# Kernel optimization log

Measured on AMD Instinct MI355X. Metric: run time of the kernel, lower is better.

The kernel has to match this reference:

```python
import jax, jax.numpy as jnp
from jax import lax
import numpy as np

B, N, NPOINT, NSAMPLE, C = 4, 8192, 2048, 32, 128
RADIUS = 0.2
H1, H2, OUT = 64, 128, 128  # mlp: (3+C)->H1->H2, sas: H2->OUT


def fps(xyz, npoint):
    # furthest point sampling: xyz (B,N,3) -> idx (B,npoint) int32
    b, n, _ = xyz.shape
    init_idx = jnp.zeros((b,), jnp.int32)

    def step(carry, _):
        dist, last = carry
        p = jnp.take_along_axis(xyz, last[:, None, None], axis=1)  # (B,1,3)
        d = jnp.sum((xyz - p) ** 2, axis=-1)                       # (B,N)
        dist = jnp.minimum(dist, d)
        nxt = jnp.argmax(dist, axis=-1).astype(jnp.int32)
        return (dist, nxt), nxt

    (_, _), rest = lax.scan(step, (jnp.full((b, n), 1e10, jnp.float32), init_idx),
                            None, length=npoint - 1)
    return jnp.concatenate([init_idx[None, :], rest], axis=0).T    # (B,npoint)


def ball_query(xyz, new_xyz, radius, nsample):
    # xyz (B,N,3), new_xyz (B,S,3) -> idx (B,S,nsample) int32
    n = xyz.shape[1]
    d2 = jnp.sum((new_xyz[:, :, None, :] - xyz[:, None, :, :]) ** 2, axis=-1)  # (B,S,N)
    ar = jnp.arange(n, dtype=jnp.int32)
    keys = jnp.where(d2 <= radius * radius, ar, n)  # valid -> own index, invalid -> N
    neg_vals, _ = lax.top_k(-keys, nsample)          # smallest nsample keys
    idx = -neg_vals
    first = idx[..., :1]
    return jnp.where(idx >= n, first, idx)           # pad invalid with first valid


def gather_points(pts, idx):
    # pts (B,N,D), idx (B,S,ns) -> (B,S,ns,D)
    b, s, ns = idx.shape
    flat = jnp.take_along_axis(pts, idx.reshape(b, s * ns, 1), axis=1)
    return flat.reshape(b, s, ns, -1)


def setup_inputs() -> dict:
    key = jax.random.key(0)
    ks = jax.random.split(key, 8)
    xyz = jax.random.uniform(ks[0], (B, N, 3), dtype=jnp.float32)
    features = jax.random.normal(ks[1], (B, C, N), dtype=jnp.float32)
    cin = C + 3
    W1 = jax.random.normal(ks[2], (H1, cin), dtype=jnp.float32) / np.sqrt(cin)
    b1 = jnp.zeros((H1,), jnp.float32)
    W2 = jax.random.normal(ks[3], (H2, H1), dtype=jnp.float32) / np.sqrt(H1)
    b2 = jnp.zeros((H2,), jnp.float32)
    Wsa = jax.random.normal(ks[4], (OUT, H2), dtype=jnp.float32) / np.sqrt(H2)
    bsa = jnp.zeros((OUT,), jnp.float32)
    return {"xyz": xyz, "features": features, "W1": W1, "b1": b1,
            "W2": W2, "b2": b2, "Wsa": Wsa, "bsa": bsa}


def reference(xyz, features, W1, b1, W2, b2, Wsa, bsa):
    center_idx = fps(xyz, NPOINT)                                   # (B,S)
    new_xyz = jnp.take_along_axis(xyz, center_idx[:, :, None], axis=1)  # (B,S,3)
    g_idx = ball_query(xyz, new_xyz, RADIUS, NSAMPLE)               # (B,S,ns)
    g_xyz = gather_points(xyz, g_idx) - new_xyz[:, :, None, :]      # (B,S,ns,3) relative coords
    g_feat = gather_points(features.transpose(0, 2, 1), g_idx)      # (B,S,ns,C)
    h = jnp.concatenate([g_xyz, g_feat], axis=-1)                   # (B,S,ns,3+C)
    h = jax.nn.relu(jnp.einsum('bsnc,oc->bsno', h, W1) + b1)        # shared 1x1-conv MLP
    h = jax.nn.relu(jnp.einsum('bsnc,oc->bsno', h, W2) + b2)
    pooled = jnp.max(h, axis=2)                                     # max over nsample -> (B,S,H2)
    out = jnp.einsum('bsc,oc->bso', pooled, Wsa) + bsa              # sas channel mixer
    return new_xyz, out.transpose(0, 2, 1)                          # (B,S,3), (B,OUT,S)
```

## Files before the change

kernel.cpp:

```cpp
#include <hip/hip_runtime.h>
#include <cstdint>
#include <cstddef>

#define NB 4
#define NN 8192
#define NPTS 2048
#define NSAMP 32
#define NC 128
#define CIN 131
#define NH1 64
#define NH2 128
#define NOUTC 128
#define GCELLS 4096

typedef float v2f __attribute__((ext_vector_type(2)));

__device__ __forceinline__ float d2_exact(float ax, float ay, float az,
                                          float bx, float by, float bz) {
  float dx = ax - bx, dy = ay - by, dz = az - bz;
  return __fadd_rn(__fadd_rn(__fmul_rn(dx, dx), __fmul_rn(dy, dy)),
                   __fmul_rn(dz, dz));
}

#if __has_builtin(__builtin_amdgcn_mov_dpp)
template <int CTRL>
__device__ __forceinline__ float dppf(float v) {
  return __int_as_float(
      __builtin_amdgcn_mov_dpp(__float_as_int(v), CTRL, 0xF, 0xF, true));
}
template <int CTRL>
__device__ __forceinline__ int dppi(int v) {
  return __builtin_amdgcn_mov_dpp(v, CTRL, 0xF, 0xF, true);
}
#else
template <int CTRL>
__device__ __forceinline__ float dppf(float v) {
  const int m = (CTRL == 0xB1) ? 1 : (CTRL == 0x4E) ? 2 : (CTRL == 0x141) ? 7 : 15;
  return __shfl_xor(v, m);
}
template <int CTRL>
__device__ __forceinline__ int dppi(int v) {
  const int m = (CTRL == 0xB1) ? 1 : (CTRL == 0x4E) ? 2 : (CTRL == 0x141) ? 7 : 15;
  return __shfl_xor(v, m);
}
#endif

__device__ __forceinline__ bool tgt(float av, int ai, float bv, int bi) {
  return (av > bv) || (av == bv && ai < bi);
}

__device__ __forceinline__ void red_pair(float& bv, int& bi, float ov, int oi) {
  bool t = tgt(ov, oi, bv, bi);
  bv = t ? ov : bv;
  bi = t ? oi : bi;
}
template <int CTRL>
__device__ __forceinline__ void red5(float& v, int& i, float& x, float& y,
                                     float& z) {
  float ov = dppf<CTRL>(v);
  int oi = dppi<CTRL>(i);
  float ox = dppf<CTRL>(x), oy = dppf<CTRL>(y), oz = dppf<CTRL>(z);
  bool t = tgt(ov, oi, v, i);
  v = t ? ov : v; i = t ? oi : i;
  x = t ? ox : x; y = t ? oy : y; z = t ? oz : z;
}

#define SEL8(A, kk, out)                      \
  {                                           \
    float s0_ = ((kk) & 1) ? A[1] : A[0];     \
    float s1_ = ((kk) & 1) ? A[3] : A[2];     \
    float s2_ = ((kk) & 1) ? A[5] : A[4];     \
    float s3_ = ((kk) & 1) ? A[7] : A[6];     \
    float s4_ = ((kk) & 2) ? s1_ : s0_;       \
    float s5_ = ((kk) & 2) ? s3_ : s2_;       \
    out = ((kk) & 4) ? s5_ : s4_;             \
  }

__device__ __forceinline__ int spread3(int v) {
  return (v & 1) | ((v & 2) << 2) | ((v & 4) << 4) | ((v & 8) << 6);
}

__global__ __launch_bounds__(1024, 1) void sort_kernel(
    const float* __restrict__ xyz, float* __restrict__ xs,
    float* __restrict__ ys, float* __restrict__ zs, int* __restrict__ io) {
  __shared__ int hist[GCELLS];
  __shared__ int cbase[GCELLS];
  __shared__ int wtot[16];
  __shared__ int woff[16];
  const int b = blockIdx.x;
  const int tid = threadIdx.x;
  const int lane = tid & 63;
  const int wid = tid >> 6;
  const float* xb = xyz + (size_t)b * NN * 3;
  for (int i = tid; i < GCELLS; i += 1024) hist[i] = 0;
  __syncthreads();
  int cell[8];
  float px[8], py[8], pz[8];
#pragma unroll
  for (int k = 0; k < 8; ++k) {
    int j = tid + (k << 10);
    float x = xb[j * 3 + 0], y = xb[j * 3 + 1], z = xb[j * 3 + 2];
    px[k] = x; py[k] = y; pz[k] = z;
    int cx = min(15, max(0, (int)(x * 16.0f)));
    int cy = min(15, max(0, (int)(y * 16.0f)));
    int cz = min(15, max(0, (int)(z * 16.0f)));
    cell[k] = spread3(cx) | (spread3(cy) << 1) | (spread3(cz) << 2);
    atomicAdd(&hist[cell[k]], 1);
  }
  __syncthreads();
  const int i0 = tid * 4;
  int h0 = hist[i0], h1 = hist[i0 + 1], h2 = hist[i0 + 2], h3 = hist[i0 + 3];
  int s4 = h0 + h1 + h2 + h3;
  int v = s4;
#pragma unroll
  for (int d = 1; d < 64; d <<= 1) {
    int o = __shfl_up(v, d);
    if (lane >= d) v += o;
  }
  if (lane == 63) wtot[wid] = v;
  __syncthreads();
  if (tid < 16) {
    int acc = 0;
    for (int w = 0; w < 16; ++w) {
      if (w == tid) woff[tid] = acc;
      acc += wtot[w];
    }
  }
  __syncthreads();
  int eb = woff[wid] + v - s4;
  cbase[i0] = eb;
  cbase[i0 + 1] = eb + h0;
  cbase[i0 + 2] = eb + h0 + h1;
  cbase[i0 + 3] = eb + h0 + h1 + h2;
  __syncthreads();
  for (int i = tid; i < GCELLS; i += 1024) hist[i] = 0;
  __syncthreads();
  const size_t bo = (size_t)b * NN;
#pragma unroll
  for (int k = 0; k < 8; ++k) {
    int pos = cbase[cell[k]] + atomicAdd(&hist[cell[k]], 1);
    xs[bo + pos] = px[k];
    ys[bo + pos] = py[k];
    zs[bo + pos] = pz[k];
    io[bo + pos] = tid + (k << 10);
  }
}

__global__ __launch_bounds__(1024, 1) void fps_kernel(
    const float* __restrict__ xyz, const float* __restrict__ xs,
    const float* __restrict__ ys, const float* __restrict__ zs,
    const int* __restrict__ io, float* __restrict__ newxyz) {
#pragma clang fp contract(off)
  const int b = blockIdx.x;
  const int tid = threadIdx.x;
  const int lane = tid & 63;
  const int wid = tid >> 6;
  const size_t bo = (size_t)b * NN;

  float X[8], Y[8], Z[8], D[8];
  int I[8];
#pragma unroll
  for (int k = 0; k < 8; ++k) {
    int s = tid * 8 + k;
    X[k] = xs[bo + s];
    Y[k] = ys[bo + s];
    Z[k] = zs[bo + s];
    I[k] = io[bo + s];
    D[k] = 1e30f;
  }

  __shared__ float sv[16];
  __shared__ int si[16];
  __shared__ float sx[16], sy[16], sz[16];
  __shared__ float fin[3];

  const float* xb = xyz + (size_t)b * NN * 3;
  float cx = xb[0], cy = xb[1], cz = xb[2];
  if (tid == 0) {
    newxyz[(size_t)b * NPTS * 3 + 0] = cx;
    newxyz[(size_t)b * NPTS * 3 + 1] = cy;
    newxyz[(size_t)b * NPTS * 3 + 2] = cz;
  }

  for (int t = 1; t < NPTS; ++t) {
    float bv = -1.0f;
    int bi = 0x7fffffff;
    int kw = 0;
#pragma unroll
    for (int k = 0; k < 8; ++k) {
      float dd = d2_exact(X[k], Y[k], Z[k], cx, cy, cz);
      float nd = fminf(D[k], dd);
      D[k] = nd;
      bool c = tgt(nd, I[k], bv, bi);
      bv = c ? nd : bv;
      bi = c ? I[k] : bi;
      kw = c ? k : kw;
    }
    float rv = bv;
    int ri = bi;
    red_pair(rv, ri, dppf<0xB1>(rv), dppi<0xB1>(ri));
    red_pair(rv, ri, dppf<0x4E>(rv), dppi<0x4E>(ri));
    red_pair(rv, ri, dppf<0x141>(rv), dppi<0x141>(ri));
    red_pair(rv, ri, dppf<0x140>(rv), dppi<0x140>(ri));
    red_pair(rv, ri, __shfl_xor(rv, 16), __shfl_xor(ri, 16));
    red_pair(rv, ri, __shfl_xor(rv, 32), __shfl_xor(ri, 32));
    if (bi == ri) {
      float ox, oy, oz;
      SEL8(X, kw, ox);
      SEL8(Y, kw, oy);
      SEL8(Z, kw, oz);
      sv[wid] = rv;
      si[wid] = ri;
      sx[wid] = ox;
      sy[wid] = oy;
      sz[wid] = oz;
    }
    __syncthreads();
    if (wid == 0) {
      const int e = lane & 15;
      float v = sv[e];
      int i = si[e];
      float xx = sx[e], yy = sy[e], zz = sz[e];
      red5<0xB1>(v, i, xx, yy, zz);
      red5<0x4E>(v, i, xx, yy, zz);
      red5<0x141>(v, i, xx, yy, zz);
      red5<0x140>(v, i, xx, yy, zz);
      if (lane == 0) {
        fin[0] = xx;
        fin[1] = yy;
        fin[2] = zz;
        size_t o = ((size_t)b * NPTS + t) * 3;
        newxyz[o + 0] = xx;
        newxyz[o + 1] = yy;
        newxyz[o + 2] = zz;
      }
    }
    __syncthreads();
    cx = fin[0];
    cy = fin[1];
    cz = fin[2];
  }
}

__global__ __launch_bounds__(1024, 1) void fps_nosort_kernel(
    const float* __restrict__ xyz, float* __restrict__ newxyz) {
#pragma clang fp contract(off)
  const int b = blockIdx.x;
  const int tid = threadIdx.x;
  const int lane = tid & 63;
  const int wid = tid >> 6;
  const float* xb = xyz + (size_t)b * NN * 3;
  v2f x2[4], y2[4], z2[4], dd[4];
#pragma unroll
  for (int p = 0; p < 4; ++p) {
    int j0 = tid + ((2 * p) << 10);
    int j1 = tid + ((2 * p + 1) << 10);
    x2[p].x = xb[j0 * 3 + 0]; x2[p].y = xb[j1 * 3 + 0];
    y2[p].x = xb[j0 * 3 + 1]; y2[p].y = xb[j1 * 3 + 1];
    z2[p].x = xb[j0 * 3 + 2]; z2[p].y = xb[j1 * 3 + 2];
    dd[p].x = 1e10f; dd[p].y = 1e10f;
  }
  __shared__ float vbuf[2][16];
  __shared__ int ibuf[2][16];
  __shared__ float cbuf[2][16][3];
  float cx = xb[0], cy = xb[1], cz = xb[2];
  if (tid == 0) {
    newxyz[(size_t)b * NPTS * 3 + 0] = cx;
    newxyz[(size_t)b * NPTS * 3 + 1] = cy;
    newxyz[(size_t)b * NPTS * 3 + 2] = cz;
  }
  for (int t = 1; t < NPTS; ++t) {
    const int par = t & 1;
    float bv = -1.0f; int bi = 0;
    float bwx = 0.f, bwy = 0.f, bwz = 0.f;
#pragma unroll
    for (int p = 0; p < 4; ++p) {
      v2f dx = x2[p] - (v2f){cx, cx};
      v2f dy = y2[p] - (v2f){cy, cy};
      v2f dz = z2[p] - (v2f){cz, cz};
      v2f s = dx * dx + dy * dy + dz * dz;
      v2f nd;
      nd.x = fminf(dd[p].x, s.x);
      nd.y = fminf(dd[p].y, s.y);
      dd[p] = nd;
      { bool c = nd.x > bv;
        bv = c ? nd.x : bv; bi = c ? (tid + ((2 * p) << 10)) : bi;
        bwx = c ? x2[p].x : bwx; bwy = c ? y2[p].x : bwy; bwz = c ? z2[p].x : bwz; }
      { bool c = nd.y > bv;
        bv = c ? nd.y : bv; bi = c ? (tid + ((2 * p + 1) << 10)) : bi;
        bwx = c ? x2[p].y : bwx; bwy = c ? y2[p].y : bwy; bwz = c ? z2[p].y : bwz; }
    }
    red_pair(bv, bi, dppf<0xB1>(bv), dppi<0xB1>(bi));
    red_pair(bv, bi, dppf<0x4E>(bv), dppi<0x4E>(bi));
    red_pair(bv, bi, dppf<0x141>(bv), dppi<0x141>(bi));
    red_pair(bv, bi, dppf<0x140>(bv), dppi<0x140>(bi));
    red_pair(bv, bi, __shfl_xor(bv, 16), __shfl_xor(bi, 16));
    red_pair(bv, bi, __shfl_xor(bv, 32), __shfl_xor(bi, 32));
    if (tid == (bi & 1023)) {
      vbuf[par][wid] = bv; ibuf[par][wid] = bi;
      cbuf[par][wid][0] = bwx; cbuf[par][wid][1] = bwy; cbuf[par][wid][2] = bwz;
    }
    __syncthreads();
    float v2w = vbuf[par][lane & 15];
    int i2w = ibuf[par][lane & 15];
    red_pair(v2w, i2w, dppf<0xB1>(v2w), dppi<0xB1>(i2w));
    red_pair(v2w, i2w, dppf<0x4E>(v2w), dppi<0x4E>(i2w));
    red_pair(v2w, i2w, dppf<0x141>(v2w), dppi<0x141>(i2w));
    red_pair(v2w, i2w, dppf<0x140>(v2w), dppi<0x140>(i2w));
    const int slot = (i2w & 1023) >> 6;
    cx = cbuf[par][slot][0]; cy = cbuf[par][slot][1]; cz = cbuf[par][slot][2];
    if (tid == (i2w & 1023)) {
      size_t o = ((size_t)b * NPTS + t) * 3;
      newxyz[o + 0] = cx; newxyz[o + 1] = cy; newxyz[o + 2] = cz;
    }
  }
}

__global__ __launch_bounds__(256) void ballq_kernel(
    const float* __restrict__ xyz, const float* __restrict__ newxyz,
    int* __restrict__ bidx) {
  const int cid = blockIdx.x * 4 + (threadIdx.x >> 6);
  const int lane = threadIdx.x & 63;
  const int b = cid >> 11;
  const float* xb = xyz + (size_t)b * NN * 3;
  const float cx = newxyz[(size_t)cid * 3 + 0];
  const float cy = newxyz[(size_t)cid * 3 + 1];
  const float cz = newxyz[(size_t)cid * 3 + 2];
  int* ob = bidx + (size_t)cid * NSAMP;
  int total = 0;
  int first = -1;
  for (int c0 = 0; c0 < NN; c0 += 64) {
    int j = c0 + lane;
    float xx = xb[j * 3 + 0], yy = xb[j * 3 + 1], zz = xb[j * 3 + 2];
    float d2 = d2_exact(cx, cy, cz, xx, yy, zz);
    bool in = d2 <= 0.04f;
    unsigned long long m = __ballot(in);
    if (first < 0 && m) first = c0 + __builtin_ctzll(m);
    int pos = total + __popcll(m & ((1ull << lane) - 1ull));
    if (in && pos < NSAMP) ob[pos] = j;
    total += __popcll(m);
    if (total >= NSAMP) break;
  }
  if (total < NSAMP && lane < NSAMP - total) ob[total + lane] = first;
}

__global__ void tw_kernel(const float* __restrict__ W1, const float* __restrict__ W2,
                          const float* __restrict__ Wsa, float* __restrict__ w1t,
                          float* __restrict__ w2t, float* __restrict__ wsat) {
  int i = blockIdx.x * blockDim.x + threadIdx.x;
  if (i < CIN * NH1) w1t[i] = W1[(i % NH1) * CIN + (i / NH1)];
  if (i < NH1 * NH2) w2t[i] = W2[(i % NH2) * NH1 + (i / NH2)];
  if (i < NH2 * NOUTC) wsat[i] = Wsa[(i % NOUTC) * NH2 + (i / NOUTC)];
}

__global__ void tfeat_kernel(const float* __restrict__ feat, float* __restrict__ featT) {
  __shared__ float tile[32][33];
  const int b = blockIdx.z;
  const int n0 = blockIdx.x * 32, c0 = blockIdx.y * 32;
  const int tx = threadIdx.x, ty = threadIdx.y;
#pragma unroll
  for (int r = 0; r < 4; ++r)
    tile[ty + r * 8][tx] = feat[((size_t)b * NC + c0 + ty + r * 8) * NN + n0 + tx];
  __syncthreads();
#pragma unroll
  for (int r = 0; r < 4; ++r)
    featT[((size_t)b * NN + n0 + ty + r * 8) * NC + c0 + tx] = tile[tx][ty + r * 8];
}

#define HS 36
__global__ __launch_bounds__(256) void mlp_kernel(
    const float* __restrict__ xyz, const float* __restrict__ fsrc,
    const float* __restrict__ newxyz, const int* __restrict__ bidx,
    const float* __restrict__ w1t, const float* __restrict__ b1,
    const float* __restrict__ w2t, const float* __restrict__ b2,
    const float* __restrict__ wsat, const float* __restrict__ bsa,
    float* __restrict__ out1, int useT) {
  __shared__ float h[CIN * HS];
  __shared__ float h1[NH1 * HS];
  __shared__ float pl[256];
  __shared__ float pooled[NH2];
  __shared__ int sidx[NSAMP];
  __shared__ float sc[3];
  const int cid = blockIdx.x;
  const int b = cid >> 11;
  const int s = cid & 2047;
  const int tid = threadIdx.x;
  if (tid < NSAMP) sidx[tid] = bidx[(size_t)cid * NSAMP + tid];
  if (tid < 3) sc[tid] = newxyz[(size_t)cid * 3 + tid];
  __syncthreads();
  {
    const int ss = tid >> 3, q = tid & 7;
    const int j = sidx[ss];
    if (useT) {
      const float4* fr = (const float4*)(fsrc + ((size_t)b * NN + j) * NC + q * 16);
#pragma unroll
      for (int u = 0; u < 4; ++u) {
        float4 v = fr[u];
        int c = 3 + q * 16 + u * 4;
        h[(c + 0) * HS + ss] = v.x;
        h[(c + 1) * HS + ss] = v.y;
        h[(c + 2) * HS + ss] = v.z;
        h[(c + 3) * HS + ss] = v.w;
      }
    } else {
      for (int u = 0; u < 16; ++u) {
        int c = q * 16 + u;
        h[(3 + c) * HS + ss] = fsrc[((size_t)b * NC + c) * NN + j];
      }
    }
    if (q == 0) {
      const float* pr = xyz + ((size_t)b * NN + j) * 3;
      h[0 * HS + ss] = pr[0] - sc[0];
      h[1 * HS + ss] = pr[1] - sc[1];
      h[2 * HS + ss] = pr[2] - sc[2];
    }
  }
  __syncthreads();
  {
    const int o = tid & 63, sg = tid >> 6;
    float acc[8];
    const float bb = b1[o];
#pragma unroll
    for (int i = 0; i < 8; ++i) acc[i] = bb;
    const float4* hb = (const float4*)&h[sg * 8];
    for (int k = 0; k < CIN; ++k) {
      float w = w1t[k * NH1 + o];
      float4 a = hb[k * (HS / 4) + 0];
      float4 c = hb[k * (HS / 4) + 1];
      acc[0] = fmaf(w, a.x, acc[0]); acc[1] = fmaf(w, a.y, acc[1]);
      acc[2] = fmaf(w, a.z, acc[2]); acc[3] = fmaf(w, a.w, acc[3]);
      acc[4] = fmaf(w, c.x, acc[4]); acc[5] = fmaf(w, c.y, acc[5]);
      acc[6] = fmaf(w, c.z, acc[6]); acc[7] = fmaf(w, c.w, acc[7]);
    }
#pragma unroll
    for (int i = 0; i < 8; ++i) h1[o * HS + sg * 8 + i] = fmaxf(acc[i], 0.0f);
  }
  __syncthreads();
  {
    const int o = tid & 127, sg = tid >> 7;
    float acc[16];
    const float bb = b2[o];
#pragma unroll
    for (int i = 0; i < 16; ++i) acc[i] = bb;
    const float4* hb = (const float4*)&h1[sg * 16];
    for (int k = 0; k < NH1; ++k) {
      float w = w2t[k * NH2 + o];
#pragma unroll
      for (int u = 0; u < 4; ++u) {
        float4 a = hb[k * (HS / 4) + u];
        acc[u * 4 + 0] = fmaf(w, a.x, acc[u * 4 + 0]);
        acc[u * 4 + 1] = fmaf(w, a.y, acc[u * 4 + 1]);
        acc[u * 4 + 2] = fmaf(w, a.z, acc[u * 4 + 2]);
        acc[u * 4 + 3] = fmaf(w, a.w, acc[u * 4 + 3]);
      }
    }
    float pm = acc[0];
#pragma unroll
    for (int i = 1; i < 16; ++i) pm = fmaxf(pm, acc[i]);
    pl[sg * 128 + o] = pm;
  }
  __syncthreads();
  if (tid < NH2) pooled[tid] = fmaxf(fmaxf(pl[tid], pl[128 + tid]), 0.0f);
  __syncthreads();
  if (tid < NOUTC) {
    float acc = bsa[tid];
    for (int k = 0; k < NH2; ++k) acc = fmaf(pooled[k], wsat[k * NOUTC + tid], acc);
    out1[((size_t)b * NOUTC + tid) * NPTS + s] = acc;
  }
}

extern "C" void kernel_launch(void* const* d_in, const int* in_sizes, int n_in,
                              void* d_out, int out_size, void* d_ws, size_t ws_size,
                              hipStream_t stream) {
  const float* xyz = (const float*)d_in[0];
  const float* feat = (const float*)d_in[1];
  const float* W1 = (const float*)d_in[2];
  const float* b1 = (const float*)d_in[3];
  const float* W2 = (const float*)d_in[4];
  const float* b2 = (const float*)d_in[5];
  const float* Wsa = (const float*)d_in[6];
  const float* bsa = (const float*)d_in[7];
  float* out = (float*)d_out;
  float* newxyz = out;
  float* out1 = out + (size_t)NB * NPTS * 3;

  const size_t sort_f = (size_t)NB * NN * 4;
  const size_t small_f = (size_t)CIN * NH1 + NH1 * NH2 + NH2 * NOUTC +
                         (size_t)NB * NPTS * NSAMP;
  const size_t featT_f = (size_t)NB * NN * NC;

  float* ws = (float*)d_ws;
  bool useSort = ws_size >= (sort_f + small_f) * 4;
  bool useT = ws_size >= (sort_f + small_f + featT_f) * 4;

  float* xs = ws;
  float* ysr = xs + (size_t)NB * NN;
  float* zsr = ysr + (size_t)NB * NN;
  int* iosr = (int*)(zsr + (size_t)NB * NN);
  float* base2 = useSort ? (ws + sort_f) : ws;
  float* w1t = base2;
  float* w2t = w1t + CIN * NH1;
  float* wsat = w2t + NH1 * NH2;
  int* bidx = (int*)(wsat + NH2 * NOUTC);
  float* featT = (float*)(bidx + (size_t)NB * NPTS * NSAMP);

  tw_kernel<<<64, 256, 0, stream>>>(W1, W2, Wsa, w1t, w2t, wsat);
  if (useT)
    tfeat_kernel<<<dim3(NN / 32, NC / 32, NB), dim3(32, 8), 0, stream>>>(feat, featT);
  if (useSort) {
    sort_kernel<<<NB, 1024, 0, stream>>>(xyz, xs, ysr, zsr, iosr);
    fps_kernel<<<NB, 1024, 0, stream>>>(xyz, xs, ysr, zsr, iosr, newxyz);
  } else {
    fps_nosort_kernel<<<NB, 1024, 0, stream>>>(xyz, newxyz);
  }
  ballq_kernel<<<NB * NPTS / 4, 256, 0, stream>>>(xyz, newxyz, bidx);
  mlp_kernel<<<NB * NPTS, 256, 0, stream>>>(xyz, useT ? featT : feat, newxyz, bidx,
                                            w1t, b1, w2t, b2, wsat, bsa, out1,
                                            (int)useT);
}
```

Measured before the change: 3.838 ms.

## Use packed 64-bit argmax keys and drop second barrier in FPS loop

Packs the distance and the inverted index into one 64-bit key, so each argmax comparison is a single unsigned compare. Every wave now does the final 16-entry cross-wave reduction redundantly from double-buffered shared memory, which removes the second __syncthreads and the broadcast through shared memory on each iteration. Coordinates are held as float2 vectors so the distance update can use packed math. The cost is more DPP/shuffle traffic for the 64-bit keys and duplicated reduction work in every wave. Correctness relies on non-negative float distances ordering correctly as unsigned bits.

```diff
diff --git a/kernel.cpp b/kernel.cpp
--- a/kernel.cpp
+++ b/kernel.cpp
@@ -14,6 +14,7 @@
 #define GCELLS 4096
 
 typedef float v2f __attribute__((ext_vector_type(2)));
+typedef unsigned long long ull;
 
 __device__ __forceinline__ float d2_exact(float ax, float ay, float az,
                                           float bx, float by, float bz) {
@@ -45,35 +46,41 @@
 }
 #endif
 
-__device__ __forceinline__ bool tgt(float av, int ai, float bv, int bi) {
-  return (av > bv) || (av == bv && ai < bi);
+template <int CTRL>
+__device__ __forceinline__ ull dppk(ull k) {
+  int hi = dppi<CTRL>((int)(k >> 32));
+  int lo = dppi<CTRL>((int)(unsigned)k);
+  return ((ull)(unsigned)hi << 32) | (unsigned)lo;
+}
+__device__ __forceinline__ ull shflk(ull k, int m) {
+  int hi = __shfl_xor((int)(k >> 32), m);
+  int lo = __shfl_xor((int)(unsigned)k, m);
+  return ((ull)(unsigned)hi << 32) | (unsigned)lo;
+}
+
+template <int CTRL>
+__device__ __forceinline__ void redk5(ull& k, float& x, float& y, float& z) {
+  ull ok = dppk<CTRL>(k);
+  float ox = dppf<CTRL>(x), oy = dppf<CTRL>(y), oz = dppf<CTRL>(z);
+  bool t = ok > k;
+  k = t ? ok : k;
+  x = t ? ox : x;
+  y = t ? oy : y;
+  z = t ? oz : z;
 }
 
 __device__ __forceinline__ void red_pair(float& bv, int& bi, float ov, int oi) {
-  bool t = tgt(ov, oi, bv, bi);
+  bool t = (ov > bv) || (ov == bv && oi < bi);
   bv = t ? ov : bv;
   bi = t ? oi : bi;
 }
-template <int CTRL>
-__device__ __forceinline__ void red5(float& v, int& i, float& x, float& y,
-                                     float& z) {
-  float ov = dppf<CTRL>(v);
-  int oi = dppi<CTRL>(i);
-  float ox = dppf<CTRL>(x), oy = dppf<CTRL>(y), oz = dppf<CTRL>(z);
-  bool t = tgt(ov, oi, v, i);
-  v = t ? ov : v; i = t ? oi : i;
-  x = t ? ox : x; y = t ? oy : y; z = t ? oz : z;
-}
-
-#define SEL8(A, kk, out)                      \
+
+#define SEL8V(A, kk, out)                     \
   {                                           \
-    float s0_ = ((kk) & 1) ? A[1] : A[0];     \
-    float s1_ = ((kk) & 1) ? A[3] : A[2];     \
-    float s2_ = ((kk) & 1) ? A[5] : A[4];     \
-    float s3_ = ((kk) & 1) ? A[7] : A[6];     \
-    float s4_ = ((kk) & 2) ? s1_ : s0_;       \
-    float s5_ = ((kk) & 2) ? s3_ : s2_;       \
-    out = ((kk) & 4) ? s5_ : s4_;             \
+    v2f t0_ = ((kk) & 2) ? A[1] : A[0];       \
+    v2f t1_ = ((kk) & 2) ? A[3] : A[2];       \
+    v2f t2_ = ((kk) & 4) ? t1_ : t0_;         \
+    out = ((kk) & 1) ? t2_.y : t2_.x;         \
   }
 
 __device__ __forceinline__ int spread3(int v) {
@@ -157,22 +164,22 @@
   const int wid = tid >> 6;
   const size_t bo = (size_t)b * NN;
 
-  float X[8], Y[8], Z[8], D[8];
-  int I[8];
-#pragma unroll
-  for (int k = 0; k < 8; ++k) {
-    int s = tid * 8 + k;
-    X[k] = xs[bo + s];
-    Y[k] = ys[bo + s];
-    Z[k] = zs[bo + s];
-    I[k] = io[bo + s];
-    D[k] = 1e30f;
-  }
-
-  __shared__ float sv[16];
-  __shared__ int si[16];
-  __shared__ float sx[16], sy[16], sz[16];
-  __shared__ float fin[3];
+  v2f X2[4], Y2[4], Z2[4], D2[4];
+  unsigned invI[8];
+#pragma unroll
+  for (int p = 0; p < 4; ++p) {
+    int s0 = tid * 8 + 2 * p, s1 = s0 + 1;
+    X2[p].x = xs[bo + s0]; X2[p].y = xs[bo + s1];
+    Y2[p].x = ys[bo + s0]; Y2[p].y = ys[bo + s1];
+    Z2[p].x = zs[bo + s0]; Z2[p].y = zs[bo + s1];
+    invI[2 * p] = ~(unsigned)io[bo + s0];
+    invI[2 * p + 1] = ~(unsigned)io[bo + s1];
+    D2[p].x = 1e30f;
+    D2[p].y = 1e30f;
+  }
+
+  __shared__ int skh[2][16], skl[2][16];
+  __shared__ float sx[2][16], sy[2][16], sz[2][16];
 
   const float* xb = xyz + (size_t)b * NN * 3;
   float cx = xb[0], cy = xb[1], cz = xb[2];
@@ -183,62 +190,64 @@
   }
 
   for (int t = 1; t < NPTS; ++t) {
-    float bv = -1.0f;
-    int bi = 0x7fffffff;
+    const int par = t & 1;
+    const v2f cxv = {cx, cx}, cyv = {cy, cy}, czv = {cz, cz};
+    ull bkey = 0ull;
     int kw = 0;
 #pragma unroll
-    for (int k = 0; k < 8; ++k) {
-      float dd = d2_exact(X[k], Y[k], Z[k], cx, cy, cz);
-      float nd = fminf(D[k], dd);
-      D[k] = nd;
-      bool c = tgt(nd, I[k], bv, bi);
-      bv = c ? nd : bv;
-      bi = c ? I[k] : bi;
-      kw = c ? k : kw;
-    }
-    float rv = bv;
-    int ri = bi;
-    red_pair(rv, ri, dppf<0xB1>(rv), dppi<0xB1>(ri));
-    red_pair(rv, ri, dppf<0x4E>(rv), dppi<0x4E>(ri));
-    red_pair(rv, ri, dppf<0x141>(rv), dppi<0x141>(ri));
-    red_pair(rv, ri, dppf<0x140>(rv), dppi<0x140>(ri));
-    red_pair(rv, ri, __shfl_xor(rv, 16), __shfl_xor(ri, 16));
-    red_pair(rv, ri, __shfl_xor(rv, 32), __shfl_xor(ri, 32));
-    if (bi == ri) {
+    for (int p = 0; p < 4; ++p) {
+      v2f dx = X2[p] - cxv;
+      v2f dy = Y2[p] - cyv;
+      v2f dz = Z2[p] - czv;
+      v2f s = dx * dx + dy * dy + dz * dz;
+      v2f nd;
+      nd.x = fminf(D2[p].x, s.x);
+      nd.y = fminf(D2[p].y, s.y);
+      D2[p] = nd;
+      ull k0 = ((ull)__float_as_uint(nd.x) << 32) | invI[2 * p];
+      bool c0 = k0 > bkey;
+      bkey = c0 ? k0 : bkey;
+      kw = c0 ? (2 * p) : kw;
+      ull k1 = ((ull)__float_as_uint(nd.y) << 32) | invI[2 * p + 1];
+      bool c1 = k1 > bkey;
+      bkey = c1 ? k1 : bkey;
+      kw = c1 ? (2 * p + 1) : kw;
+    }
+    ull rk = bkey;
+    { ull o = dppk<0xB1>(rk);  rk = o > rk ? o : rk; }
+    { ull o = dppk<0x4E>(rk);  rk = o > rk ? o : rk; }
+    { ull o = dppk<0x141>(rk); rk = o > rk ? o : rk; }
+    { ull o = dppk<0x140>(rk); rk = o > rk ? o : rk; }
+    { ull o = shflk(rk, 16);   rk = o > rk ? o : rk; }
+    { ull o = shflk(rk, 32);   rk = o > rk ? o : rk; }
+    if (bkey == rk) {
       float ox, oy, oz;
-      SEL8(X, kw, ox);
-      SEL8(Y, kw, oy);
-      SEL8(Z, kw, oz);
-      sv[wid] = rv;
-      si[wid] = ri;
-      sx[wid] = ox;
-      sy[wid] = oy;
-      sz[wid] = oz;
+      SEL8V(X2, kw, ox);
+      SEL8V(Y2, kw, oy);
+      SEL8V(Z2, kw, oz);
+      skh[par][wid] = (int)(rk >> 32);
+      skl[par][wid] = (int)(unsigned)rk;
+      sx[par][wid] = ox;
+      sy[par][wid] = oy;
+      sz[par][wid] = oz;
     }
     __syncthreads();
-    if (wid == 0) {
-      const int e = lane & 15;
-      float v = sv[e];
-      int i = si[e];
-      float xx = sx[e], yy = sy[e], zz = sz[e];
-      red5<0xB1>(v, i, xx, yy, zz);
-      red5<0x4E>(v, i, xx, yy, zz);
-      red5<0x141>(v, i, xx, yy, zz);
-      red5<0x140>(v, i, xx, yy, zz);
-      if (lane == 0) {
-        fin[0] = xx;
-        fin[1] = yy;
-        fin[2] = zz;
-        size_t o = ((size_t)b * NPTS + t) * 3;
-        newxyz[o + 0] = xx;
-        newxyz[o + 1] = yy;
-        newxyz[o + 2] = zz;
-      }
-    }
-    __syncthreads();
-    cx = fin[0];
-    cy = fin[1];
-    cz = fin[2];
+    const int sl = lane & 15;
+    ull mk = ((ull)(unsigned)skh[par][sl] << 32) | (unsigned)skl[par][sl];
+    float xx = sx[par][sl], yy = sy[par][sl], zz = sz[par][sl];
+    redk5<0xB1>(mk, xx, yy, zz);
+    redk5<0x4E>(mk, xx, yy, zz);
+    redk5<0x141>(mk, xx, yy, zz);
+    redk5<0x140>(mk, xx, yy, zz);
+    cx = xx;
+    cy = yy;
+    cz = zz;
+    if (tid == 0) {
+      size_t o = ((size_t)b * NPTS + t) * 3;
+      newxyz[o + 0] = xx;
+      newxyz[o + 1] = yy;
+      newxyz[o + 2] = zz;
+    }
   }
 }
 
```

After: 3.679 ms. 1.04x faster.
